# Performance work log

Hardware: AMD Instinct MI355X
Metric: run time of the kernel (lower is better)

## Reference

```python
import jax, jax.numpy as jnp
import numpy as np
import math

B, L, D = 4, 4096, 64

def setup_inputs() -> dict:
    key = jax.random.key(0)
    kq, kk, kv = jax.random.split(key, 3)
    q = jax.random.normal(kq, (B, L, D), dtype=jnp.float32)
    k = jax.random.normal(kk, (B, L, D), dtype=jnp.float32)
    v = jax.random.normal(kv, (B, L, D), dtype=jnp.float32)
    return {"q": q, "k": k, "v": v}

def reference(q, k, v):
    d_model = k.shape[-1]
    # score[b,i,j] = <q_i, k_j> / sqrt(d)   -> [B, L, L]
    score = jnp.einsum('bid,bjd->bij', q, k) / math.sqrt(d_model)
    attn = jax.nn.softmax(score.astype(jnp.float32), axis=-1)
    # Faithful to source: output = (v^T @ attn)^T = attn^T @ v
    # output[b,j,d] = sum_i attn[b,i,j] * v[b,i,d]
    out = jnp.einsum('bij,bid->bjd', attn, v)
    return out
```

## Files before the change

### kernel.cpp

```cpp
#include <hip/hip_runtime.h>
#include <hip/hip_bf16.h>

#define LQ 4096
#define DD 64
#define NB 4
#define NTOT ((size_t)NB * LQ * DD)
#define NROW ((size_t)NB * LQ)
#define NJC 16

typedef __attribute__((ext_vector_type(4))) float f32x4;
typedef __attribute__((ext_vector_type(8))) short short8;
typedef __attribute__((ext_vector_type(4))) short short4v;
typedef __attribute__((ext_vector_type(2))) unsigned int uint2v;
typedef __attribute__((ext_vector_type(4))) unsigned short ushort4v;

static __device__ __forceinline__ unsigned short f2bf(float x) {
  __hip_bfloat16 h = __float2bfloat16(x);
  return __builtin_bit_cast(unsigned short, h);
}
static __device__ __forceinline__ float ex2(float x) { return __builtin_amdgcn_exp2f(x); }

static __device__ __forceinline__ f32x4 mfma16(short4v a, short4v b, f32x4 c) {
#if __has_builtin(__builtin_amdgcn_mfma_f32_16x16x16bf16_1k)
  return __builtin_amdgcn_mfma_f32_16x16x16bf16_1k(a, b, c, 0, 0, 0);
#else
  asm volatile("v_mfma_f32_16x16x16_bf16 %0, %1, %2, %0"
               : "+v"(c) : "v"(a), "v"(b));
  return c;
#endif
}

#define C1 0.18033688011112042f


__global__ __launch_bounds__(256) void prep_kernel(
    const float* __restrict__ q, const float* __restrict__ k,
    unsigned short* __restrict__ Qf, unsigned short* __restrict__ Kf)
{
  __shared__ __align__(16) unsigned short tile[64][72];
  const int bx = blockIdx.x;
  const int b = bx >> 6, s = bx & 63;
  const int tid = threadIdx.x;
  const int r = tid >> 2, c0 = (tid & 3) << 4;
  const int w = tid >> 6, lane = tid & 63;
  const int l15 = lane & 15, g = lane >> 4;
  const size_t rowbase = ((size_t)b * LQ + s * 64 + r) * DD + c0;
  const size_t bbase = (size_t)b * LQ * DD;

#pragma unroll
  for (int arr = 0; arr < 2; ++arr) {
    const float* src = arr ? k : q;
    unsigned short* dst = arr ? Kf : Qf;
    ushort4v o[4];
#pragma unroll
    for (int e = 0; e < 4; ++e) {
      const f32x4 x = *(const f32x4*)(src + rowbase + e * 4);
      o[e] = (ushort4v){ f2bf(x[0]), f2bf(x[1]), f2bf(x[2]), f2bf(x[3]) };
    }
    if (arr) __syncthreads();
#pragma unroll
    for (int e = 0; e < 4; ++e) *(ushort4v*)(&tile[r][c0 + e * 4]) = o[e];
    __syncthreads();
    const int T = s * 4 + w;
#pragma unroll
    for (int kh = 0; kh < 2; ++kh) {
      const unsigned short* pp = &tile[w * 16 + l15][kh * 32 + g * 8];
      const ushort4v lo = *(const ushort4v*)pp;
      const ushort4v hi = *(const ushort4v*)(pp + 4);
      unsigned short* od = dst + bbase + (((size_t)T * 2 + kh) * 64 + lane) * 8;
      *(ushort4v*)od = lo;
      *(ushort4v*)(od + 4) = hi;
    }
  }
}

__global__ __launch_bounds__(256) void stats_kernel(
    const unsigned short* __restrict__ Qf, const unsigned short* __restrict__ Kf,
    float* __restrict__ part_ls)
{
  const int bx = blockIdx.x;
  const int x = bx & 7, kk = bx >> 3;
  const int b = x >> 1;
  const int jc = ((x & 1) << 3) + (kk >> 4);
  const int it = kk & 15;
  const int tid = threadIdx.x, w = tid >> 6, lane = tid & 63;
  const int l15 = lane & 15, g = lane >> 4;
  const size_t bbase = (size_t)b * LQ * DD;
  const unsigned short* Qp = Qf + bbase;
  const unsigned short* Kp = Kf + bbase;

  short8 aq[4][2];
#pragma unroll
  for (int is = 0; is < 4; ++is)
#pragma unroll
    for (int kh = 0; kh < 2; ++kh) {
      const int T = it * 16 + w * 4 + is;
      aq[is][kh] = *(const short8*)(Qp + (((size_t)T * 2 + kh) * 64 + lane) * 8);
    }

  float ls[4][4];
#pragma unroll
  for (int is = 0; is < 4; ++is)
#pragma unroll
    for (int qq = 0; qq < 4; ++qq) ls[is][qq] = 0.f;

  const int J0 = jc * 16;
  short8 kf[3][2];
#pragma unroll
  for (int pb = 0; pb < 2; ++pb)
#pragma unroll
    for (int kh = 0; kh < 2; ++kh)
      kf[pb][kh] = *(const short8*)(Kp + (((size_t)(J0 + pb) * 2 + kh) * 64 + lane) * 8);

#pragma unroll
  for (int itr = 0; itr < 16; ++itr) {
    const int buf = itr % 3;
    if (itr + 2 < 16) {
      const int nb2 = (itr + 2) % 3;
#pragma unroll
      for (int kh = 0; kh < 2; ++kh)
        kf[nb2][kh] = *(const short8*)(Kp + (((size_t)(J0 + itr + 2) * 2 + kh) * 64 + lane) * 8);
    }
#pragma unroll
    for (int is = 0; is < 4; ++is) {
      f32x4 tt = __builtin_amdgcn_mfma_f32_16x16x32_bf16(
          aq[is][0], kf[buf][0], (f32x4){0.f, 0.f, 0.f, 0.f}, 0, 0, 0);
      tt = __builtin_amdgcn_mfma_f32_16x16x32_bf16(aq[is][1], kf[buf][1], tt, 0, 0, 0);
#pragma unroll
      for (int qq = 0; qq < 4; ++qq) ls[is][qq] += ex2(tt[qq] * C1);
    }
  }
#pragma unroll
  for (int mask = 1; mask <= 8; mask <<= 1)
#pragma unroll
    for (int is = 0; is < 4; ++is)
#pragma unroll
      for (int qq = 0; qq < 4; ++qq) ls[is][qq] += __shfl_xor(ls[is][qq], mask, 64);
  if (l15 == 0) {
#pragma unroll
    for (int is = 0; is < 4; ++is) {
      const int T = it * 16 + w * 4 + is;
#pragma unroll
      for (int qq = 0; qq < 4; ++qq)
        part_ls[(size_t)jc * NROW + b * LQ + T * 16 + g * 4 + qq] = ls[is][qq];
    }
  }
}

__global__ __launch_bounds__(256) void combine_kernel(
    const float* __restrict__ part_ls, const float* __restrict__ v,
    unsigned short* __restrict__ Vf)
{
  __shared__ __align__(16) unsigned short tile[64][72];
  const int bx = blockIdx.x;
  const int b = bx >> 6, s = bx & 63;
  const int tid = threadIdx.x;
  const int r = tid >> 2, c0 = (tid & 3) << 4;
  const int w = tid >> 6, lane = tid & 63;
  const int l15 = lane & 15, g = lane >> 4;
  const int row = b * LQ + s * 64 + r;

  float l = 0.f;
#pragma unroll
  for (int jc = 0; jc < NJC; ++jc) l += part_ls[(size_t)jc * NROW + row];
  const float sc = 1.0f / l;

  const size_t rowbase = (size_t)row * DD + c0;
#pragma unroll
  for (int e = 0; e < 4; ++e) {
    const f32x4 xv = *(const f32x4*)(v + rowbase + e * 4);
    ushort4v o = { f2bf(xv[0] * sc), f2bf(xv[1] * sc),
                   f2bf(xv[2] * sc), f2bf(xv[3] * sc) };
    *(ushort4v*)(&tile[r][c0 + e * 4]) = o;
  }
  __syncthreads();
  const int T = s * 4 + w;
  const size_t bbase = (size_t)b * LQ * DD;
#pragma unroll
  for (int dp = 0; dp < 2; ++dp) {
    ushort4v lo, hi;
#pragma unroll
    for (int c = 0; c < 4; ++c) {
      lo[c] = tile[w * 16 + g * 4 + c][(2 * dp) * 16 + l15];
      hi[c] = tile[w * 16 + g * 4 + c][(2 * dp + 1) * 16 + l15];
    }
    unsigned short* od = Vf + bbase + (((size_t)T * 2 + dp) * 64 + lane) * 8;
    *(ushort4v*)od = lo;
    *(ushort4v*)(od + 4) = hi;
  }
}

__global__ __launch_bounds__(1024) void attn_out_kernel(
    const unsigned short* __restrict__ Qf, const unsigned short* __restrict__ Kf,
    const unsigned short* __restrict__ Vf, float* __restrict__ out)
{
  __shared__ float red[16 * 2048];

  const int bx = blockIdx.x;
  const int x = bx & 7;
  const int b = x >> 1;
  const int jt = ((x & 1) << 5) + (bx >> 3);
  const int tid = threadIdx.x, w = tid >> 6, lane = tid & 63;
  const int p = w >> 1, sub = w & 1;
  const int l15 = lane & 15, g = lane >> 4;

  const size_t bbase = (size_t)b * LQ * DD;
  const unsigned short* Qp = Qf + bbase;
  const unsigned short* Kp = Kf + bbase;
  const unsigned short* Vp = Vf + bbase;

  short8 ka[2][2];
#pragma unroll
  for (int jsl = 0; jsl < 2; ++jsl)
#pragma unroll
    for (int kh = 0; kh < 2; ++kh) {
      const int JT = jt * 4 + sub * 2 + jsl;
      ka[jsl][kh] = *(const short8*)(Kp + (((size_t)JT * 2 + kh) * 64 + lane) * 8);
    }

  f32x4 acc[2][4];
#pragma unroll
  for (int jsl = 0; jsl < 2; ++jsl)
#pragma unroll
    for (int ds = 0; ds < 4; ++ds) acc[jsl][ds] = (f32x4){0.f, 0.f, 0.f, 0.f};

  const int T0 = p * 32;
  short8 qb[3][2], vb[3][2];
#pragma unroll
  for (int pb = 0; pb < 2; ++pb) {
#pragma unroll
    for (int kh = 0; kh < 2; ++kh)
      qb[pb][kh] = *(const short8*)(Qp + (((size_t)(T0 + pb) * 2 + kh) * 64 + lane) * 8);
#pragma unroll
    for (int dp = 0; dp < 2; ++dp)
      vb[pb][dp] = *(const short8*)(Vp + (((size_t)(T0 + pb) * 2 + dp) * 64 + lane) * 8);
  }

#pragma unroll
  for (int itr = 0; itr < 32; ++itr) {
    const int buf = itr % 3;
    if (itr + 2 < 32) {
      const int nb2 = (itr + 2) % 3;
      const int Tn = T0 + itr + 2;
#pragma unroll
      for (int kh = 0; kh < 2; ++kh)
        qb[nb2][kh] = *(const short8*)(Qp + (((size_t)Tn * 2 + kh) * 64 + lane) * 8);
#pragma unroll
      for (int dp = 0; dp < 2; ++dp)
        vb[nb2][dp] = *(const short8*)(Vp + (((size_t)Tn * 2 + dp) * 64 + lane) * 8);
    }

    union VU { short8 s8; short4v s4[2]; } vu0, vu1;
    vu0.s8 = vb[buf][0];
    vu1.s8 = vb[buf][1];

    __builtin_amdgcn_s_setprio(1);
#pragma unroll
    for (int jsl = 0; jsl < 2; ++jsl) {
      f32x4 tt = __builtin_amdgcn_mfma_f32_16x16x32_bf16(
          qb[buf][0], ka[jsl][0], (f32x4){0.f, 0.f, 0.f, 0.f}, 0, 0, 0);
      tt = __builtin_amdgcn_mfma_f32_16x16x32_bf16(qb[buf][1], ka[jsl][1], tt, 0, 0, 0);
      const unsigned a0 = __builtin_bit_cast(unsigned, ex2(tt[0] * C1)) + 0x8000u;
      const unsigned a1 = __builtin_bit_cast(unsigned, ex2(tt[1] * C1)) + 0x8000u;
      const unsigned a2 = __builtin_bit_cast(unsigned, ex2(tt[2] * C1)) + 0x8000u;
      const unsigned a3 = __builtin_bit_cast(unsigned, ex2(tt[3] * C1)) + 0x8000u;
      uint2v uu;
      uu[0] = __builtin_amdgcn_perm(a1, a0, 0x07060302u);
      uu[1] = __builtin_amdgcn_perm(a3, a2, 0x07060302u);
      const short4v pa = __builtin_bit_cast(short4v, uu);
      acc[jsl][0] = mfma16(pa, vu0.s4[0], acc[jsl][0]);
      acc[jsl][1] = mfma16(pa, vu0.s4[1], acc[jsl][1]);
      acc[jsl][2] = mfma16(pa, vu1.s4[0], acc[jsl][2]);
      acc[jsl][3] = mfma16(pa, vu1.s4[1], acc[jsl][3]);
    }
    __builtin_amdgcn_s_setprio(0);
  }

  __syncthreads();
#pragma unroll
  for (int jsl = 0; jsl < 2; ++jsl)
#pragma unroll
    for (int ds = 0; ds < 4; ++ds)
#pragma unroll
      for (int qq = 0; qq < 4; ++qq)
        red[w * 2048 + (jsl * 16 + g * 4 + qq) * 64 + ds * 16 + l15] = acc[jsl][ds][qq];
  __syncthreads();
  {
    float* op = out + ((size_t)b * LQ + jt * 64) * DD;
#pragma unroll
    for (int rr = 0; rr < 4; ++rr) {
      const int r = w * 4 + rr;
      const int sr = r >> 5, rl = r & 31;
      float s = 0.f;
#pragma unroll
      for (int pp = 0; pp < 8; ++pp)
        s += red[(pp * 2 + sr) * 2048 + rl * 64 + lane];
      op[r * 64 + lane] = s;
    }
  }
}

extern "C" void kernel_launch(void* const* d_in, const int* in_sizes, int n_in,
                              void* d_out, int out_size, void* d_ws, size_t ws_size,
                              hipStream_t stream) {
  const float* q = (const float*)d_in[0];
  const float* k = (const float*)d_in[1];
  const float* v = (const float*)d_in[2];

  unsigned short* Qf = (unsigned short*)d_ws;
  unsigned short* Kf = Qf + NTOT;
  unsigned short* Vf = Kf + NTOT;
  float* part_ls = (float*)(Vf + NTOT);
  float* outp = (float*)d_out;

  prep_kernel<<<NB * 64, 256, 0, stream>>>(q, k, Qf, Kf);
  stats_kernel<<<1024, 256, 0, stream>>>(Qf, Kf, part_ls);
  combine_kernel<<<NB * 64, 256, 0, stream>>>(part_ls, v, Vf);
  attn_out_kernel<<<256, 1024, 0, stream>>>(Qf, Kf, Vf, outp);
}
```

Measured before the change: 52.47 us.

## Halve attn_out block size so each wave owns four key tiles and reuses Q/V loads

The attention-output kernel now runs with 512 threads (8 waves) instead of 1024. Each wave processes all four 16-column key subtiles over a 32-tile stretch of queries, instead of two subtiles. This halves the redundant Q/V fragment loads per block and shrinks the cross-wave reduction from 16 to 8 partials. The final reduction is also vectorised with float4 LDS reads and stores. In exchange each wave holds twice as many accumulators, raising register pressure, and there are fewer waves per block to hide latency, though launch bounds request two blocks per CU.

```diff
diff --git a/kernel.cpp b/kernel.cpp
--- a/kernel.cpp
+++ b/kernel.cpp
@@ -190,18 +190,17 @@
   }
 }
 
-__global__ __launch_bounds__(1024) void attn_out_kernel(
+__global__ __launch_bounds__(512, 2) void attn_out_kernel(
     const unsigned short* __restrict__ Qf, const unsigned short* __restrict__ Kf,
     const unsigned short* __restrict__ Vf, float* __restrict__ out)
 {
-  __shared__ float red[16 * 2048];
+  __shared__ float red[8 * 4096];
 
   const int bx = blockIdx.x;
   const int x = bx & 7;
   const int b = x >> 1;
   const int jt = ((x & 1) << 5) + (bx >> 3);
   const int tid = threadIdx.x, w = tid >> 6, lane = tid & 63;
-  const int p = w >> 1, sub = w & 1;
   const int l15 = lane & 15, g = lane >> 4;
 
   const size_t bbase = (size_t)b * LQ * DD;
@@ -209,22 +208,22 @@
   const unsigned short* Kp = Kf + bbase;
   const unsigned short* Vp = Vf + bbase;
 
-  short8 ka[2][2];
-#pragma unroll
-  for (int jsl = 0; jsl < 2; ++jsl)
+  short8 ka[4][2];
+#pragma unroll
+  for (int js = 0; js < 4; ++js)
 #pragma unroll
     for (int kh = 0; kh < 2; ++kh) {
-      const int JT = jt * 4 + sub * 2 + jsl;
-      ka[jsl][kh] = *(const short8*)(Kp + (((size_t)JT * 2 + kh) * 64 + lane) * 8);
-    }
-
-  f32x4 acc[2][4];
-#pragma unroll
-  for (int jsl = 0; jsl < 2; ++jsl)
-#pragma unroll
-    for (int ds = 0; ds < 4; ++ds) acc[jsl][ds] = (f32x4){0.f, 0.f, 0.f, 0.f};
-
-  const int T0 = p * 32;
+      const int JT = jt * 4 + js;
+      ka[js][kh] = *(const short8*)(Kp + (((size_t)JT * 2 + kh) * 64 + lane) * 8);
+    }
+
+  f32x4 acc[4][4];
+#pragma unroll
+  for (int js = 0; js < 4; ++js)
+#pragma unroll
+    for (int ds = 0; ds < 4; ++ds) acc[js][ds] = (f32x4){0.f, 0.f, 0.f, 0.f};
+
+  const int T0 = w * 32;
   short8 qb[3][2], vb[3][2];
 #pragma unroll
   for (int pb = 0; pb < 2; ++pb) {
@@ -256,10 +255,10 @@
 
     __builtin_amdgcn_s_setprio(1);
 #pragma unroll
-    for (int jsl = 0; jsl < 2; ++jsl) {
+    for (int js = 0; js < 4; ++js) {
       f32x4 tt = __builtin_amdgcn_mfma_f32_16x16x32_bf16(
-          qb[buf][0], ka[jsl][0], (f32x4){0.f, 0.f, 0.f, 0.f}, 0, 0, 0);
-      tt = __builtin_amdgcn_mfma_f32_16x16x32_bf16(qb[buf][1], ka[jsl][1], tt, 0, 0, 0);
+          qb[buf][0], ka[js][0], (f32x4){0.f, 0.f, 0.f, 0.f}, 0, 0, 0);
+      tt = __builtin_amdgcn_mfma_f32_16x16x32_bf16(qb[buf][1], ka[js][1], tt, 0, 0, 0);
       const unsigned a0 = __builtin_bit_cast(unsigned, ex2(tt[0] * C1)) + 0x8000u;
       const unsigned a1 = __builtin_bit_cast(unsigned, ex2(tt[1] * C1)) + 0x8000u;
       const unsigned a2 = __builtin_bit_cast(unsigned, ex2(tt[2] * C1)) + 0x8000u;
@@ -268,35 +267,38 @@
       uu[0] = __builtin_amdgcn_perm(a1, a0, 0x07060302u);
       uu[1] = __builtin_amdgcn_perm(a3, a2, 0x07060302u);
       const short4v pa = __builtin_bit_cast(short4v, uu);
-      acc[jsl][0] = mfma16(pa, vu0.s4[0], acc[jsl][0]);
-      acc[jsl][1] = mfma16(pa, vu0.s4[1], acc[jsl][1]);
-      acc[jsl][2] = mfma16(pa, vu1.s4[0], acc[jsl][2]);
-      acc[jsl][3] = mfma16(pa, vu1.s4[1], acc[jsl][3]);
+      acc[js][0] = mfma16(pa, vu0.s4[0], acc[js][0]);
+      acc[js][1] = mfma16(pa, vu0.s4[1], acc[js][1]);
+      acc[js][2] = mfma16(pa, vu1.s4[0], acc[js][2]);
+      acc[js][3] = mfma16(pa, vu1.s4[1], acc[js][3]);
     }
     __builtin_amdgcn_s_setprio(0);
   }
 
   __syncthreads();
 #pragma unroll
-  for (int jsl = 0; jsl < 2; ++jsl)
+  for (int js = 0; js < 4; ++js)
 #pragma unroll
     for (int ds = 0; ds < 4; ++ds)
 #pragma unroll
       for (int qq = 0; qq < 4; ++qq)
-        red[w * 2048 + (jsl * 16 + g * 4 + qq) * 64 + ds * 16 + l15] = acc[jsl][ds][qq];
+        red[w * 4096 + (js * 16 + g * 4 + qq) * 64 + ds * 16 + l15] = acc[js][ds][qq];
   __syncthreads();
   {
     float* op = out + ((size_t)b * LQ + jt * 64) * DD;
-#pragma unroll
-    for (int rr = 0; rr < 4; ++rr) {
-      const int r = w * 4 + rr;
-      const int sr = r >> 5, rl = r & 31;
-      float s = 0.f;
-#pragma unroll
-      for (int pp = 0; pp < 8; ++pp)
-        s += red[(pp * 2 + sr) * 2048 + rl * 64 + lane];
-      op[r * 64 + lane] = s;
-    }
+    const int jj = tid >> 3;
+    const int d0 = (tid & 7) << 3;
+    f32x4 s0 = (f32x4){0.f, 0.f, 0.f, 0.f};
+    f32x4 s1 = (f32x4){0.f, 0.f, 0.f, 0.f};
+#pragma unroll
+    for (int u = 0; u < 8; ++u) {
+      const f32x4 t0 = *(const f32x4*)&red[u * 4096 + jj * 64 + d0];
+      const f32x4 t1 = *(const f32x4*)&red[u * 4096 + jj * 64 + d0 + 4];
+      s0[0] += t0[0]; s0[1] += t0[1]; s0[2] += t0[2]; s0[3] += t0[3];
+      s1[0] += t1[0]; s1[1] += t1[1]; s1[2] += t1[2]; s1[3] += t1[3];
+    }
+    *(f32x4*)(op + jj * 64 + d0) = s0;
+    *(f32x4*)(op + jj * 64 + d0 + 4) = s1;
   }
 }
 
@@ -316,5 +318,5 @@
   prep_kernel<<<NB * 64, 256, 0, stream>>>(q, k, Qf, Kf);
   stats_kernel<<<1024, 256, 0, stream>>>(Qf, Kf, part_ls);
   combine_kernel<<<NB * 64, 256, 0, stream>>>(part_ls, v, Vf);
-  attn_out_kernel<<<256, 1024, 0, stream>>>(Qf, Kf, Vf, outp);
-}
+  attn_out_kernel<<<256, 512, 0, stream>>>(Qf, Kf, Vf, outp);
+}
```

New measurement: 51.57 us. Within noise of the previous version (-1.7%).
